# Optimization experiments

Measured on AMD Instinct MI355X. Metric: run time of the kernel, lower is better.

## Reference

```python
import jax, jax.numpy as jnp
import numpy as np

N_NODES = 50000
N_EDGES = 600000
EMB_DIM = 128
NUM_LAYERS = 5
NUM_ELEM = 118
NUM_CHIR = 4
NUM_BOND_TYPE = 4
NUM_BOND_DIR = 3
BN_EPS = 1e-5


def _xavier(key, shape):
    fan_in, fan_out = shape[0], shape[1]
    limit = np.sqrt(6.0 / (fan_in + fan_out))
    return jax.random.uniform(key, shape, jnp.float32, -limit, limit)


def setup_inputs() -> dict:
    key = jax.random.key(0)
    ks = jax.random.split(key, 12)
    x = jax.random.randint(ks[0], (N_NODES, 2), 0, 4, dtype=jnp.int64)
    edge_index = jax.random.randint(ks[1], (2, N_EDGES), 0, N_NODES, dtype=jnp.int64)
    edge_attr = jax.random.randint(ks[2], (N_EDGES, 2), 0, 3, dtype=jnp.int64)
    elem_emb = _xavier(ks[3], (NUM_ELEM, EMB_DIM))
    chir_emb = _xavier(ks[4], (NUM_CHIR, EMB_DIM))
    bond_type_emb = _xavier(ks[5], (NUM_BOND_TYPE, EMB_DIM))
    bond_dir_emb = _xavier(ks[6], (NUM_BOND_DIR, EMB_DIM))
    # shared GINEConv MLP: Linear(D, 2D) -> ReLU -> Linear(2D, D)
    W1 = _xavier(ks[7], (EMB_DIM, 2 * EMB_DIM))
    b1 = jnp.zeros((2 * EMB_DIM,), jnp.float32)
    W2 = _xavier(ks[8], (2 * EMB_DIM, EMB_DIM))
    b2 = jnp.zeros((EMB_DIM,), jnp.float32)
    # per-layer BatchNorm affine params
    bn_gamma = jnp.ones((NUM_LAYERS, EMB_DIM), jnp.float32)
    bn_beta = jnp.zeros((NUM_LAYERS, EMB_DIM), jnp.float32)
    return {
        "x": x, "edge_index": edge_index, "edge_attr": edge_attr,
        "elem_emb": elem_emb, "chir_emb": chir_emb,
        "bond_type_emb": bond_type_emb, "bond_dir_emb": bond_dir_emb,
        "W1": W1, "b1": b1, "W2": W2, "b2": b2,
        "bn_gamma": bn_gamma, "bn_beta": bn_beta,
    }


def reference(x, edge_index, edge_attr, elem_emb, chir_emb,
              bond_type_emb, bond_dir_emb, W1, b1, W2, b2,
              bn_gamma, bn_beta):
    # input embeddings
    h = elem_emb[x[:, 0]] + chir_emb[x[:, 1]]                    # [N, D]
    e = bond_type_emb[edge_attr[:, 0]] + bond_dir_emb[edge_attr[:, 1]]  # [E, D]
    src, dst = edge_index[0], edge_index[1]
    n = h.shape[0]
    num_layers = bn_gamma.shape[0]
    for layer in range(num_layers):  # conv weights shared across layers
        # GINEConv: msg = relu(x_j + edge_attr), scatter-add, eps=0
        msg = jax.nn.relu(h[src] + e)                            # [E, D]
        agg = jax.ops.segment_sum(msg, dst, num_segments=n)      # [N, D]
        z = h + agg
        out = jax.nn.relu(z @ W1 + b1) @ W2 + b2                 # [N, D]
        # BatchNorm1d (training mode: batch stats, biased variance)
        mean = out.mean(axis=0)
        var = out.var(axis=0)
        out = (out - mean) * jax.lax.rsqrt(var + BN_EPS) * bn_gamma[layer] + bn_beta[layer]
        h = out if layer == num_layers - 1 else jax.nn.relu(out)
    return h
```

## Files before the change

### kernel.cpp

```cpp
#include <hip/hip_runtime.h>

typedef _Float16 f16;
typedef _Float16 f16x8 __attribute__((ext_vector_type(8)));
typedef _Float16 h2 __attribute__((ext_vector_type(2)));
typedef float f32x4 __attribute__((ext_vector_type(4)));
typedef unsigned short u16;
typedef unsigned int u32;

__device__ __forceinline__ float bf2f(u16 b) {
  union { u32 u; float f; } t; t.u = ((u32)b) << 16; return t.f;
}
__device__ __forceinline__ u16 f2bf(float f) {
  union { float f; u32 u; } t; t.f = f;
  u32 u = t.u;
  return (u16)((u + 0x7FFFu + ((u >> 16) & 1u)) >> 16);
}
__device__ __forceinline__ u16 f2h_bits(float f) {
  f16 h = (f16)f;
  union { f16 h; u16 u; } t; t.h = h; return t.u;
}
__device__ __forceinline__ float2 up2(u32 p) {
  union { u32 u; f16 h[2]; } t; t.u = p;
  float2 r; r.x = (float)t.h[0]; r.y = (float)t.h[1]; return r;
}
__device__ __forceinline__ u32 pk2(float x, float y) {
  return (u32)f2h_bits(x) | ((u32)f2h_bits(y) << 16);
}
__device__ __forceinline__ h2 asH2(u32 u) {
  union { u32 u; h2 h; } t; t.u = u; return t.h;
}
__device__ __forceinline__ h2 relu2(h2 a) {
#if __has_builtin(__builtin_elementwise_max)
  h2 z = {(_Float16)0, (_Float16)0};
  return __builtin_elementwise_max(a, z);
#else
  h2 r;
  r.x = a.x > (_Float16)0 ? a.x : (_Float16)0;
  r.y = a.y > (_Float16)0 ? a.y : (_Float16)0;
  return r;
#endif
}

__global__ void k_detect(const u16* __restrict__ elemRaw, const int* __restrict__ eiRaw,
                         int* __restrict__ dflags) {
  __shared__ int bad, nzOdd;
  if (threadIdx.x == 0) { bad = 0; nzOdd = 0; }
  __syncthreads();
  int myBad = 0;
  for (int i = threadIdx.x; i < 4096; i += 256) {
    float v = bf2f(elemRaw[i]);
    if (!(v > -0.2f && v < 0.2f)) myBad++;
  }
  if (myBad) atomicAdd(&bad, myBad);
  int myNz = 0;
  for (int i = threadIdx.x; i < 1024; i += 256)
    if (eiRaw[2 * i + 1] != 0) myNz++;
  if (myNz) atomicAdd(&nzOdd, myNz);
  __syncthreads();
  if (threadIdx.x == 0) {
    dflags[0] = (bad == 0) ? 1 : 0;
    dflags[1] = (nzOdd > 16) ? 1 : 0;
  }
}

__global__ void k_canary(u32* __restrict__ out, const int* __restrict__ dflags,
                         int out_size, u32 pBf, u32 pF32) {
  int isbf = dflags[0];
  int words = isbf ? (out_size >> 1) : out_size;
  int i = blockIdx.x * 256 + threadIdx.x;
  if (i < words) out[i] = isbf ? pBf : pF32;
}

__global__ void k_zero(int* counts, float* stats, int NPad) {
  int i = blockIdx.x * blockDim.x + threadIdx.x;
  if (i < NPad) counts[i] = 0;
  else if (i < NPad + 1280) stats[i - NPad] = 0.f;
}

__global__ void k_cvt(const int* __restrict__ xR, const int* __restrict__ eiR,
                      const int* __restrict__ eaR,
                      const u16* e0, const u16* e1, const u16* e2, const u16* e3,
                      const u16* e4, const u16* e5, const u16* e6, const u16* e7,
                      const u16* e8, const u16* e9,
                      const int* __restrict__ dflags,
                      int* __restrict__ x32, int* __restrict__ ei32, int* __restrict__ combo,
                      int* __restrict__ counts, float* __restrict__ dst,
                      int N, int E, int intBlocks) {
  if ((int)blockIdx.x < intBlocks) {
    int pi = blockIdx.x * 256 + threadIdx.x;
    int nPairs = N + 2 * E;
    if (pi >= nPairs) return;
    int is32 = dflags[1];
    const int* src; int local; int kind;
    if (pi < N) { src = xR; local = pi; kind = 0; }
    else if (pi < N + E) { src = eiR; local = pi - N; kind = 1; }
    else { src = eaR; local = pi - N - E; kind = 2; }
    int j0 = 2 * local;
    int v0, v1;
    if (is32) { int2 v = *(const int2*)(src + j0); v0 = v.x; v1 = v.y; }
    else      { int4 v = *(const int4*)(src + 2 * j0); v0 = v.x; v1 = v.z; }
    if (kind == 0) { x32[j0] = v0; x32[j0 + 1] = v1; }
    else if (kind == 1) {
      ei32[j0] = v0; ei32[j0 + 1] = v1;
      if (j0 >= E) {
        atomicAdd(&counts[v0], 1);
        atomicAdd(&counts[v1], 1);
      }
    } else {
      combo[local] = v0 * 3 + v1;
    }
  } else {
    int i = (blockIdx.x - intBlocks) * 256 + threadIdx.x;
    if (i >= 83712) return;
    int isbf = dflags[0];
    const u16* src; int j;
    if      (i < 15104) { src = e0; j = i; }
    else if (i < 15616) { src = e1; j = i - 15104; }
    else if (i < 16128) { src = e2; j = i - 15616; }
    else if (i < 16512) { src = e3; j = i - 16128; }
    else if (i < 49280) { src = e4; j = i - 16512; }
    else if (i < 49536) { src = e5; j = i - 49280; }
    else if (i < 82304) { src = e6; j = i - 49536; }
    else if (i < 82432) { src = e7; j = i - 82304; }
    else if (i < 83072) { src = e8; j = i - 82432; }
    else                { src = e9; j = i - 83072; }
    dst[i] = isbf ? bf2f(src[j]) : ((const float*)src)[j];
  }
}

__global__ void k_chunksum(const int* __restrict__ counts, int* __restrict__ bsum) {
  int tid = threadIdx.x, lane = tid & 63, w = tid >> 6;
  const int4* c4 = (const int4*)(counts + blockIdx.x * 1024);
  int4 v = c4[tid];
  int s = v.x + v.y + v.z + v.w;
#pragma unroll
  for (int d = 1; d < 64; d <<= 1) s += __shfl_xor(s, d);
  __shared__ int ws[4];
  if (lane == 0) ws[w] = s;
  __syncthreads();
  if (tid == 0) bsum[blockIdx.x] = ws[0] + ws[1] + ws[2] + ws[3];
}

__global__ void k_chunkscan(const int* __restrict__ bsum, int* __restrict__ boff,
                            int* __restrict__ row_start, int N, int nCh) {
  int t = threadIdx.x;
  int v = (t < nCh) ? bsum[t] : 0;
  int incl = v;
#pragma unroll
  for (int d = 1; d < 64; d <<= 1) { int tmp = __shfl_up(incl, d); if (t >= d) incl += tmp; }
  boff[t] = incl - v;
  if (t == 63) row_start[N] = incl;
}

__global__ void k_scanapply(const int* __restrict__ counts, const int* __restrict__ boff,
                            int* __restrict__ row_start, int* __restrict__ cursor, int N) {
  int tid = threadIdx.x, lane = tid & 63, w = tid >> 6;
  int base = blockIdx.x * 1024 + tid * 4;
  int4 v = *(const int4*)(counts + base);
  int tsum = v.x + v.y + v.z + v.w;
  int incl = tsum;
#pragma unroll
  for (int d = 1; d < 64; d <<= 1) { int tmp = __shfl_up(incl, d); if (lane >= d) incl += tmp; }
  __shared__ int ws[4];
  if (lane == 63) ws[w] = incl;
  __syncthreads();
  int woff = 0;
  for (int j = 0; j < w; ++j) woff += ws[j];
  int excl = boff[blockIdx.x] + woff + incl - tsum;
  int e0 = excl, e1 = excl + v.x, e2 = e1 + v.y, e3 = e2 + v.z;
  if (base < N)     { row_start[base] = e0;     cursor[base] = e0; }
  if (base + 1 < N) { row_start[base + 1] = e1; cursor[base + 1] = e1; }
  if (base + 2 < N) { row_start[base + 2] = e2; cursor[base + 2] = e2; }
  if (base + 3 < N) { row_start[base + 3] = e3; cursor[base + 3] = e3; }
}

__global__ void k_scatter(const int* __restrict__ ei, const int* __restrict__ combo,
                          int* cursor, int* packed, int E) {
  int e = blockIdx.x * blockDim.x + threadIdx.x;
  if (e >= E) return;
  int s = ei[e], d = ei[E + e];
  int cb = combo[e];
  int pos = atomicAdd(&cursor[d], 1);
  packed[pos] = s | (cb << 20);
}

__global__ void k_prep(const float* __restrict__ cflt, const int* __restrict__ x,
                       u16* W1T, u16* W2T, u32* __restrict__ tblC,
                       u32* __restrict__ hb, int N, int wtBlocks) {
  if ((int)blockIdx.x < wtBlocks) {
    const float* W1 = cflt + 16512;
    const float* W2 = cflt + 49536;
    const float* bt = cflt + 15616;
    const float* bd = cflt + 16128;
    int g = blockIdx.x * 256 + threadIdx.x;
    int k1 = g >> 8, n1 = g & 255;
    W1T[n1 * 128 + k1] = f2h_bits(W1[g]);
    int k2 = g >> 7, n2 = g & 127;
    W2T[n2 * 256 + k2] = f2h_bits(W2[g]);
    if (g < 768) {
      int combo = g >> 6, l = g & 63, c0 = l * 2;
      int a0 = combo / 3, a1 = combo - a0 * 3;
      tblC[g] = pk2(bt[a0 * 128 + c0] + bd[a1 * 128 + c0],
                    bt[a0 * 128 + c0 + 1] + bd[a1 * 128 + c0 + 1]);
    }
  } else {
    const float* elem = cflt;
    const float* chir = cflt + 15104;
    int b = blockIdx.x - wtBlocks;
    int wv = (int)(threadIdx.x >> 6);
    int lane = threadIdx.x & 63;
    int node = b * 4 + wv;
    if (node >= N) return;
    int x0 = x[node * 2], x1 = x[node * 2 + 1];
    int c0 = lane * 2;
    float vx = elem[x0 * 128 + c0] + chir[x1 * 128 + c0];
    float vy = elem[x0 * 128 + c0 + 1] + chir[x1 * 128 + c0 + 1];
    hb[(size_t)node * 64 + lane] = pk2(vx, vy);
  }
}

__global__ __launch_bounds__(256) void k_agg(
    const u32* __restrict__ hb, const int* __restrict__ row_start,
    const int* __restrict__ packed, const u32* __restrict__ tblC,
    u32* __restrict__ z, int N, int Mpad) {
  __shared__ u32 tbl[12 * 64];
  for (int idx = threadIdx.x; idx < 768; idx += 256) tbl[idx] = tblC[idx];
  __syncthreads();
  int wv = __builtin_amdgcn_readfirstlane((int)(threadIdx.x >> 6));
  int lane = threadIdx.x & 63;
  int node = blockIdx.x * 4 + wv;
  if (node >= Mpad) return;
  if (node >= N) { z[(size_t)node * 64 + lane] = 0u; return; }
  float2 sv = up2(hb[(size_t)node * 64 + lane]);
  float accx = sv.x, accy = sv.y;
  int s_ = row_start[node], e_ = row_start[node + 1];
  int p = s_;
  for (; p + 4 <= e_; p += 4) {
    int k0 = packed[p], k1 = packed[p + 1], k2 = packed[p + 2], k3 = packed[p + 3];
    u32 r0 = hb[(size_t)(k0 & 0xFFFFF) * 64 + lane];
    u32 r1 = hb[(size_t)(k1 & 0xFFFFF) * 64 + lane];
    u32 r2 = hb[(size_t)(k2 & 0xFFFFF) * 64 + lane];
    u32 r3 = hb[(size_t)(k3 & 0xFFFFF) * 64 + lane];
    u32 t0 = tbl[(k0 >> 20) * 64 + lane];
    u32 t1 = tbl[(k1 >> 20) * 64 + lane];
    u32 t2 = tbl[(k2 >> 20) * 64 + lane];
    u32 t3 = tbl[(k3 >> 20) * 64 + lane];
    h2 m0 = relu2(asH2(r0) + asH2(t0));
    h2 m1 = relu2(asH2(r1) + asH2(t1));
    h2 m2 = relu2(asH2(r2) + asH2(t2));
    h2 m3 = relu2(asH2(r3) + asH2(t3));
    accx += (float)m0.x + (float)m1.x + (float)m2.x + (float)m3.x;
    accy += (float)m0.y + (float)m1.y + (float)m2.y + (float)m3.y;
  }
  for (; p < e_; ++p) {
    int k0 = packed[p];
    u32 r0 = hb[(size_t)(k0 & 0xFFFFF) * 64 + lane];
    u32 t0 = tbl[(k0 >> 20) * 64 + lane];
    h2 m0 = relu2(asH2(r0) + asH2(t0));
    accx += (float)m0.x;
    accy += (float)m0.y;
  }
  z[(size_t)node * 64 + lane] = pk2(accx, accy);
}

__global__ __launch_bounds__(256) void k_mlp(
    const u16* __restrict__ z, const u16* __restrict__ W1T, const u16* __restrict__ W2T,
    const float* __restrict__ b1, const float* __restrict__ b2,
    u16* __restrict__ act, float* __restrict__ statsL, int N) {
  __shared__ u16 sZ[64 * 128];
  __shared__ u16 sW1[64 * 128];
  __shared__ u16 sW2[128 * 64];
  __shared__ u16 sY[64 * 64];
  __shared__ float sRed[2][2][128];

  const int tid = threadIdx.x;
  const int w = tid >> 6, lane = tid & 63;
  const int lo = lane & 15, q = lane >> 4;
  const int r0 = (w & 1) * 32;
  const int c0w = (w >> 1) * 32;
  const int n20 = (w >> 1) * 64;
  const int row0 = blockIdx.x * 64;

#pragma unroll
  for (int t = 0; t < 4; ++t) {
    int L = t * 4096 + tid * 16;
    int row = L >> 8, slot = (L >> 4) & 15;
    int kb = slot ^ (row & 15);
    int4 v = *(const int4*)((const char*)z + (size_t)(row0 + row) * 256 + kb * 16);
    *(int4*)((char*)sZ + L) = v;
  }
#pragma unroll
  for (int t = 0; t < 4; ++t) {
    int L = t * 4096 + tid * 16;
    int n = L >> 8, slot = (L >> 4) & 15;
    int kb = slot ^ (n & 15);
    *(int4*)((char*)sW1 + L) =
        *(const int4*)((const char*)W1T + (size_t)n * 256 + kb * 16);
  }
#pragma unroll
  for (int t = 0; t < 4; ++t) {
    int L = t * 4096 + tid * 16;
    int n = L >> 7, slot = (L >> 4) & 7;
    int kb = slot ^ (n & 7);
    *(int4*)((char*)sW2 + L) =
        *(const int4*)((const char*)W2T + (size_t)n * 512 + kb * 16);
  }
  __syncthreads();

  f16x8 a[4][2];
#pragma unroll
  for (int ks = 0; ks < 4; ++ks) {
    int kq = ks * 4 + q;
#pragma unroll
    for (int rt = 0; rt < 2; ++rt) {
      int row = r0 + rt * 16 + lo;
      a[ks][rt] = *(const f16x8*)(sZ + row * 128 + ((kq ^ (row & 15)) << 3));
    }
  }

  f32x4 accO[2][4] = {};
  for (int c = 0; c < 4; ++c) {
    if (c) {
      __syncthreads();
#pragma unroll
      for (int t = 0; t < 4; ++t) {
        int L = t * 4096 + tid * 16;
        int n = L >> 8, slot = (L >> 4) & 15;
        int kb = slot ^ (n & 15);
        *(int4*)((char*)sW1 + L) =
            *(const int4*)((const char*)W1T + (size_t)(c * 64 + n) * 256 + kb * 16);
      }
#pragma unroll
      for (int t = 0; t < 4; ++t) {
        int L = t * 4096 + tid * 16;
        int n = L >> 7, slot = (L >> 4) & 7;
        int kb = slot ^ (n & 7);
        *(int4*)((char*)sW2 + L) =
            *(const int4*)((const char*)W2T + (size_t)n * 512 + c * 128 + kb * 16);
      }
      __syncthreads();
    }

    f32x4 acc1[2][2] = {};
#pragma unroll
    for (int ks = 0; ks < 4; ++ks) {
      int kq = ks * 4 + q;
      f16x8 b[2];
#pragma unroll
      for (int nt = 0; nt < 2; ++nt) {
        int n = c0w + nt * 16 + lo;
        b[nt] = *(const f16x8*)(sW1 + n * 128 + ((kq ^ (n & 15)) << 3));
      }
#pragma unroll
      for (int rt = 0; rt < 2; ++rt)
#pragma unroll
        for (int nt = 0; nt < 2; ++nt)
          acc1[rt][nt] = __builtin_amdgcn_mfma_f32_16x16x32_f16(a[ks][rt], b[nt], acc1[rt][nt], 0, 0, 0);
    }

#pragma unroll
    for (int nt = 0; nt < 2; ++nt) {
      int kcol = c0w + nt * 16 + lo;
      float bias = b1[c * 64 + kcol];
#pragma unroll
      for (int rt = 0; rt < 2; ++rt)
#pragma unroll
        for (int i = 0; i < 4; ++i) {
          int m = r0 + rt * 16 + q * 4 + i;
          float v = fmaxf(acc1[rt][nt][i] + bias, 0.f);
          sY[m * 64 + (((kcol >> 3) ^ (m & 7)) << 3) + (kcol & 7)] = f2h_bits(v);
        }
    }
    __syncthreads();

#pragma unroll
    for (int ks2 = 0; ks2 < 2; ++ks2) {
      int kq = ks2 * 4 + q;
      f16x8 a2[2], bb[4];
#pragma unroll
      for (int rt = 0; rt < 2; ++rt) {
        int m = r0 + rt * 16 + lo;
        a2[rt] = *(const f16x8*)(sY + m * 64 + ((kq ^ (m & 7)) << 3));
      }
#pragma unroll
      for (int nt = 0; nt < 4; ++nt) {
        int n = n20 + nt * 16 + lo;
        bb[nt] = *(const f16x8*)(sW2 + n * 64 + ((kq ^ (n & 7)) << 3));
      }
#pragma unroll
      for (int rt = 0; rt < 2; ++rt)
#pragma unroll
        for (int nt = 0; nt < 4; ++nt)
          accO[rt][nt] = __builtin_amdgcn_mfma_f32_16x16x32_f16(a2[rt], bb[nt], accO[rt][nt], 0, 0, 0);
    }
  }

#pragma unroll
  for (int nt = 0; nt < 4; ++nt) {
    int n2 = n20 + nt * 16 + lo;
    float bias = b2[n2];
    float ssum = 0.f, ssq = 0.f;
#pragma unroll
    for (int rt = 0; rt < 2; ++rt)
#pragma unroll
      for (int i = 0; i < 4; ++i) {
        int row = row0 + r0 + rt * 16 + q * 4 + i;
        float v = accO[rt][nt][i] + bias;
        act[(size_t)row * 128 + n2] = f2h_bits(v);
        if (row < N) { ssum += v; ssq += v * v; }
      }
    ssum += __shfl_xor(ssum, 16); ssum += __shfl_xor(ssum, 32);
    ssq  += __shfl_xor(ssq, 16);  ssq  += __shfl_xor(ssq, 32);
    if (q == 0) { sRed[w & 1][0][n2] = ssum; sRed[w & 1][1][n2] = ssq; }
  }
  __syncthreads();
  {
    int col = tid & 127, which = (tid >> 7) & 1;
    atomicAdd(&statsL[which * 128 + col], sRed[0][which][col] + sRed[1][which][col]);
  }
}

__global__ __launch_bounds__(256) void k_bnapply(
    const u32* __restrict__ act, const float* __restrict__ statsL,
    const float* __restrict__ gamma, const float* __restrict__ beta,
    float invN, u32* __restrict__ hb, int N) {
  __shared__ float ssc[128], ssh[128];
  int tid = threadIdx.x;
  if (tid < 128) {
    float mean = statsL[tid] * invN;
    float var = statsL[128 + tid] * invN - mean * mean;
    float inv = rsqrtf(var + 1e-5f);
    float scv = gamma[tid] * inv;
    ssc[tid] = scv;
    ssh[tid] = beta[tid] - mean * scv;
  }
  __syncthreads();
  int total = N * 64;
  for (int i = blockIdx.x * 256 + tid; i < total; i += gridDim.x * 256) {
    int c0 = (i & 63) * 2;
    float2 v = up2(act[i]);
    float ox = fmaxf(v.x * ssc[c0] + ssh[c0], 0.f);
    float oy = fmaxf(v.y * ssc[c0 + 1] + ssh[c0 + 1], 0.f);
    hb[i] = pk2(ox, oy);
  }
}

__global__ __launch_bounds__(256) void k_final(
    const u32* __restrict__ act, const float* __restrict__ statsL,
    const float* __restrict__ gamma, const float* __restrict__ beta,
    float invN, const int* __restrict__ dflags, void* __restrict__ outv, int N) {
  __shared__ float ssc[128], ssh[128];
  int tid = threadIdx.x;
  if (tid < 128) {
    float mean = statsL[tid] * invN;
    float var = statsL[128 + tid] * invN - mean * mean;
    float inv = rsqrtf(var + 1e-5f);
    float scv = gamma[tid] * inv;
    ssc[tid] = scv;
    ssh[tid] = beta[tid] - mean * scv;
  }
  __syncthreads();
  int isbf = dflags[0];
  int total = N * 64;
  for (int i = blockIdx.x * 256 + tid; i < total; i += gridDim.x * 256) {
    int c0 = (i & 63) * 2;
    float2 v = up2(act[i]);
    float ox = v.x * ssc[c0] + ssh[c0];
    float oy = v.y * ssc[c0 + 1] + ssh[c0 + 1];
    if (isbf) ((u32*)outv)[i] = (u32)f2bf(ox) | ((u32)f2bf(oy) << 16);
    else { float2 o; o.x = ox; o.y = oy; ((float2*)outv)[i] = o; }
  }
}

extern "C" void kernel_launch(void* const* d_in, const int* in_sizes, int n_in,
                              void* d_out, int out_size, void* d_ws, size_t ws_size,
                              hipStream_t stream) {
  const int* xR  = (const int*)d_in[0];
  const int* eiR = (const int*)d_in[1];
  const int* eaR = (const int*)d_in[2];
  const u16* emR = (const u16*)d_in[3];
  const u16* chR = (const u16*)d_in[4];
  const u16* btR = (const u16*)d_in[5];
  const u16* bdR = (const u16*)d_in[6];
  const u16* W1R = (const u16*)d_in[7];
  const u16* b1R = (const u16*)d_in[8];
  const u16* W2R = (const u16*)d_in[9];
  const u16* b2R = (const u16*)d_in[10];
  const u16* gR  = (const u16*)d_in[11];
  const u16* beR = (const u16*)d_in[12];

  const int N = in_sizes[0] / 2;
  const int E = in_sizes[1] / 2;
  const int L = in_sizes[11] / 128;
  const int Mpad = ((N + 63) / 64) * 64;
  const int nCh = (N + 1023) / 1024;
  const int NPad = nCh * 1024;

  char* base = (char*)d_ws;
  size_t off = 0;
  auto take = [&](size_t bytes) -> void* {
    void* p = base + off;
    off += (bytes + 255) & ~(size_t)255;
    return p;
  };
  int*   dflags    = (int*)  take(256);
  int*   x32       = (int*)  take((size_t)2 * N * 4);
  int*   ei32      = (int*)  take((size_t)2 * E * 4);
  int*   combo     = (int*)  take((size_t)E * 4);
  float* cflt      = (float*)take(83712 * 4);
  u32*   act       = (u32*)  take((size_t)Mpad * 64 * 4);
  u32*   hb        = (u32*)  take((size_t)Mpad * 64 * 4);
  u16*   zb        = (u16*)  take((size_t)Mpad * 128 * 2);
  int*   packed    = (int*)  take((size_t)E * 4);
  int*   row_start = (int*)  take((size_t)(N + 1) * 4);
  int*   cursor    = (int*)  take((size_t)N * 4);
  int*   counts    = (int*)  take((size_t)NPad * 4);
  int*   bsum      = (int*)  take(64 * 4);
  int*   boff      = (int*)  take(64 * 4);
  float* stats     = (float*)take((size_t)L * 256 * 4);
  u16*   W1T       = (u16*)  take(32768 * 2);
  u16*   W2T       = (u16*)  take(32768 * 2);
  u32*   tblC      = (u32*)  take(768 * 4);
  const size_t need = off;
  (void)n_in;

  float* cB1 = cflt + 49280;
  float* cB2 = cflt + 82304;
  float* cGamma = cflt + 82432;
  float* cBeta = cflt + 83072;

  k_detect<<<dim3(1), dim3(256), 0, stream>>>(emR, eiR, dflags);

  if (need > ws_size) {
    k_canary<<<dim3((out_size + 255) / 256), dim3(256), 0, stream>>>(
        (u32*)d_out, dflags, out_size, 0x40004000u, 0x40000000u);
    return;
  }

  k_zero<<<dim3((NPad + 1280 + 255) / 256), dim3(256), 0, stream>>>(counts, stats, NPad);

  const int nPairs = N + 2 * E;
  const int intBlocks = (nPairs + 255) / 256;
  const int fltBlocks = (83712 + 255) / 256;
  k_cvt<<<dim3(intBlocks + fltBlocks), dim3(256), 0, stream>>>(
      xR, eiR, eaR, emR, chR, btR, bdR, W1R, b1R, W2R, b2R, gR, beR,
      dflags, x32, ei32, combo, counts, cflt, N, E, intBlocks);

  k_chunksum<<<dim3(nCh), dim3(256), 0, stream>>>(counts, bsum);
  k_chunkscan<<<dim3(1), dim3(64), 0, stream>>>(bsum, boff, row_start, N, nCh);
  k_scanapply<<<dim3(nCh), dim3(256), 0, stream>>>(counts, boff, row_start, cursor, N);
  k_scatter<<<dim3((E + 255) / 256), dim3(256), 0, stream>>>(ei32, combo, cursor, packed, E);

  const int wtBlocks = 128;
  k_prep<<<dim3(wtBlocks + (N + 3) / 4), dim3(256), 0, stream>>>(
      cflt, x32, W1T, W2T, tblC, hb, N, wtBlocks);

  const float invN = 1.0f / (float)N;
  for (int l = 0; l < L; ++l) {
    k_agg<<<dim3(Mpad / 4), dim3(256), 0, stream>>>(
        hb, row_start, packed, tblC, (u32*)zb, N, Mpad);
    k_mlp<<<dim3(Mpad / 64), dim3(256), 0, stream>>>(
        zb, W1T, W2T, cB1, cB2, (u16*)act, stats + (size_t)l * 256, N);
    if (l < L - 1) {
      k_bnapply<<<dim3(1024), dim3(256), 0, stream>>>(
          act, stats + (size_t)l * 256, cGamma + (size_t)l * 128, cBeta + (size_t)l * 128,
          invN, hb, N);
    }
  }
  k_final<<<dim3(1024), dim3(256), 0, stream>>>(
      act, stats + (size_t)(L - 1) * 256, cGamma + (size_t)(L - 1) * 128,
      cBeta + (size_t)(L - 1) * 128, invN, dflags, d_out, N);
}
```

Measured before the change: 521.5 us.

## Fuse BatchNorm apply into aggregation gather and prefetch MLP weights into registers

Removes the separate BN-apply kernel. The aggregation kernel now computes the previous layer's scale and shift and applies normalize+ReLU in fp16 to each gathered neighbour row and to the self row, with a -inf clamp on layer 0 to act as identity. This drops one full read/write pass over node features per layer and one launch, but repeats the normalization on every edge (about 12x more FMAs) and does it in half precision. Separately, the MLP kernel preloads the next weight chunk into registers while the current chunk computes, which overlaps global loads with MFMA work at the cost of extra registers.

```diff
diff --git a/kernel.cpp b/kernel.cpp
--- a/kernel.cpp
+++ b/kernel.cpp
@@ -29,14 +29,13 @@
 __device__ __forceinline__ h2 asH2(u32 u) {
   union { u32 u; h2 h; } t; t.u = u; return t.h;
 }
-__device__ __forceinline__ h2 relu2(h2 a) {
+__device__ __forceinline__ h2 maxh2(h2 a, h2 b) {
 #if __has_builtin(__builtin_elementwise_max)
-  h2 z = {(_Float16)0, (_Float16)0};
-  return __builtin_elementwise_max(a, z);
+  return __builtin_elementwise_max(a, b);
 #else
   h2 r;
-  r.x = a.x > (_Float16)0 ? a.x : (_Float16)0;
-  r.y = a.y > (_Float16)0 ? a.y : (_Float16)0;
+  r.x = a.x > b.x ? a.x : b.x;
+  r.y = a.y > b.y ? a.y : b.y;
   return r;
 #endif
 }
@@ -186,7 +185,7 @@
 
 __global__ void k_prep(const float* __restrict__ cflt, const int* __restrict__ x,
                        u16* W1T, u16* W2T, u32* __restrict__ tblC,
-                       u32* __restrict__ hb, int N, int wtBlocks) {
+                       u32* __restrict__ act, int N, int wtBlocks) {
   if ((int)blockIdx.x < wtBlocks) {
     const float* W1 = cflt + 16512;
     const float* W2 = cflt + 49536;
@@ -215,48 +214,70 @@
     int c0 = lane * 2;
     float vx = elem[x0 * 128 + c0] + chir[x1 * 128 + c0];
     float vy = elem[x0 * 128 + c0 + 1] + chir[x1 * 128 + c0 + 1];
-    hb[(size_t)node * 64 + lane] = pk2(vx, vy);
+    act[(size_t)node * 64 + lane] = pk2(vx, vy);
   }
 }
 
 __global__ __launch_bounds__(256) void k_agg(
-    const u32* __restrict__ hb, const int* __restrict__ row_start,
+    const u32* __restrict__ act, const int* __restrict__ row_start,
     const int* __restrict__ packed, const u32* __restrict__ tblC,
+    const float* __restrict__ statsPrev, const float* __restrict__ gammaPrev,
+    const float* __restrict__ betaPrev, float invN, int l0,
     u32* __restrict__ z, int N, int Mpad) {
-  __shared__ u32 tbl[12 * 64];
-  for (int idx = threadIdx.x; idx < 768; idx += 256) tbl[idx] = tblC[idx];
+  __shared__ u32 tbl[768];
+  __shared__ u32 sscp[64], sshp[64];
+  int tid = threadIdx.x;
+  for (int idx = tid; idx < 768; idx += 256) tbl[idx] = tblC[idx];
+  if (tid < 64) {
+    float sc0 = 1.f, sc1 = 1.f, sh0 = 0.f, sh1 = 0.f;
+    if (!l0) {
+      int c0 = tid * 2;
+      float m0 = statsPrev[c0] * invN, m1 = statsPrev[c0 + 1] * invN;
+      float v0 = statsPrev[128 + c0] * invN - m0 * m0;
+      float v1 = statsPrev[128 + c0 + 1] * invN - m1 * m1;
+      float i0 = rsqrtf(v0 + 1e-5f), i1 = rsqrtf(v1 + 1e-5f);
+      sc0 = gammaPrev[c0] * i0; sc1 = gammaPrev[c0 + 1] * i1;
+      sh0 = betaPrev[c0] - m0 * sc0; sh1 = betaPrev[c0 + 1] - m1 * sc1;
+    }
+    sscp[tid] = pk2(sc0, sc1);
+    sshp[tid] = pk2(sh0, sh1);
+  }
   __syncthreads();
   int wv = __builtin_amdgcn_readfirstlane((int)(threadIdx.x >> 6));
   int lane = threadIdx.x & 63;
   int node = blockIdx.x * 4 + wv;
   if (node >= Mpad) return;
   if (node >= N) { z[(size_t)node * 64 + lane] = 0u; return; }
-  float2 sv = up2(hb[(size_t)node * 64 + lane]);
-  float accx = sv.x, accy = sv.y;
+  u32 limu = l0 ? 0xFC00FC00u : 0u;
+  h2 sc2 = asH2(sscp[lane]), sh2 = asH2(sshp[lane]);
+  h2 lim = asH2(limu), zero2 = asH2(0u);
+  h2 aa = asH2(act[(size_t)node * 64 + lane]);
+  h2 tt = maxh2(aa * sc2 + sh2, lim);
+  float accx = (float)tt.x, accy = (float)tt.y;
   int s_ = row_start[node], e_ = row_start[node + 1];
   int p = s_;
   for (; p + 4 <= e_; p += 4) {
     int k0 = packed[p], k1 = packed[p + 1], k2 = packed[p + 2], k3 = packed[p + 3];
-    u32 r0 = hb[(size_t)(k0 & 0xFFFFF) * 64 + lane];
-    u32 r1 = hb[(size_t)(k1 & 0xFFFFF) * 64 + lane];
-    u32 r2 = hb[(size_t)(k2 & 0xFFFFF) * 64 + lane];
-    u32 r3 = hb[(size_t)(k3 & 0xFFFFF) * 64 + lane];
+    u32 r0 = act[(size_t)(k0 & 0xFFFFF) * 64 + lane];
+    u32 r1 = act[(size_t)(k1 & 0xFFFFF) * 64 + lane];
+    u32 r2 = act[(size_t)(k2 & 0xFFFFF) * 64 + lane];
+    u32 r3 = act[(size_t)(k3 & 0xFFFFF) * 64 + lane];
     u32 t0 = tbl[(k0 >> 20) * 64 + lane];
     u32 t1 = tbl[(k1 >> 20) * 64 + lane];
     u32 t2 = tbl[(k2 >> 20) * 64 + lane];
     u32 t3 = tbl[(k3 >> 20) * 64 + lane];
-    h2 m0 = relu2(asH2(r0) + asH2(t0));
-    h2 m1 = relu2(asH2(r1) + asH2(t1));
-    h2 m2 = relu2(asH2(r2) + asH2(t2));
-    h2 m3 = relu2(asH2(r3) + asH2(t3));
+    h2 m0 = maxh2(maxh2(asH2(r0) * sc2 + sh2, lim) + asH2(t0), zero2);
+    h2 m1 = maxh2(maxh2(asH2(r1) * sc2 + sh2, lim) + asH2(t1), zero2);
+    h2 m2 = maxh2(maxh2(asH2(r2) * sc2 + sh2, lim) + asH2(t2), zero2);
+    h2 m3 = maxh2(maxh2(asH2(r3) * sc2 + sh2, lim) + asH2(t3), zero2);
     accx += (float)m0.x + (float)m1.x + (float)m2.x + (float)m3.x;
     accy += (float)m0.y + (float)m1.y + (float)m2.y + (float)m3.y;
   }
   for (; p < e_; ++p) {
     int k0 = packed[p];
-    u32 r0 = hb[(size_t)(k0 & 0xFFFFF) * 64 + lane];
+    u32 r0 = act[(size_t)(k0 & 0xFFFFF) * 64 + lane];
     u32 t0 = tbl[(k0 >> 20) * 64 + lane];
-    h2 m0 = relu2(asH2(r0) + asH2(t0));
+    h2 m0 = maxh2(maxh2(asH2(r0) * sc2 + sh2, lim) + asH2(t0), zero2);
     accx += (float)m0.x;
     accy += (float)m0.y;
   }
@@ -281,64 +302,61 @@
   const int n20 = (w >> 1) * 64;
   const int row0 = blockIdx.x * 64;
 
+  const char* W1b = (const char*)W1T;
+  const char* W2b = (const char*)W2T;
+  int L_[4], b1o[4], b2o[4];
 #pragma unroll
   for (int t = 0; t < 4; ++t) {
     int L = t * 4096 + tid * 16;
+    L_[t] = L;
+    int n1 = L >> 8, s1 = (L >> 4) & 15;
+    b1o[t] = n1 * 256 + (s1 ^ (n1 & 15)) * 16;
+    int n2 = L >> 7, s2 = (L >> 4) & 7;
+    b2o[t] = n2 * 512 + (s2 ^ (n2 & 7)) * 16;
+  }
+  int4 rW1[4], rW2[4];
+#pragma unroll
+  for (int t = 0; t < 4; ++t) {
+    rW1[t] = *(const int4*)(W1b + b1o[t]);
+    rW2[t] = *(const int4*)(W2b + b2o[t]);
+  }
+#pragma unroll
+  for (int t = 0; t < 4; ++t) {
+    int L = L_[t];
     int row = L >> 8, slot = (L >> 4) & 15;
     int kb = slot ^ (row & 15);
     int4 v = *(const int4*)((const char*)z + (size_t)(row0 + row) * 256 + kb * 16);
     *(int4*)((char*)sZ + L) = v;
   }
-#pragma unroll
-  for (int t = 0; t < 4; ++t) {
-    int L = t * 4096 + tid * 16;
-    int n = L >> 8, slot = (L >> 4) & 15;
-    int kb = slot ^ (n & 15);
-    *(int4*)((char*)sW1 + L) =
-        *(const int4*)((const char*)W1T + (size_t)n * 256 + kb * 16);
-  }
-#pragma unroll
-  for (int t = 0; t < 4; ++t) {
-    int L = t * 4096 + tid * 16;
-    int n = L >> 7, slot = (L >> 4) & 7;
-    int kb = slot ^ (n & 7);
-    *(int4*)((char*)sW2 + L) =
-        *(const int4*)((const char*)W2T + (size_t)n * 512 + kb * 16);
-  }
-  __syncthreads();
 
   f16x8 a[4][2];
-#pragma unroll
-  for (int ks = 0; ks < 4; ++ks) {
-    int kq = ks * 4 + q;
-#pragma unroll
-    for (int rt = 0; rt < 2; ++rt) {
-      int row = r0 + rt * 16 + lo;
-      a[ks][rt] = *(const f16x8*)(sZ + row * 128 + ((kq ^ (row & 15)) << 3));
-    }
-  }
-
   f32x4 accO[2][4] = {};
+#pragma unroll
   for (int c = 0; c < 4; ++c) {
-    if (c) {
-      __syncthreads();
+    if (c) __syncthreads();
+#pragma unroll
+    for (int t = 0; t < 4; ++t) {
+      *(int4*)((char*)sW1 + L_[t]) = rW1[t];
+      *(int4*)((char*)sW2 + L_[t]) = rW2[t];
+    }
+    __syncthreads();
+    if (c < 3) {
 #pragma unroll
       for (int t = 0; t < 4; ++t) {
-        int L = t * 4096 + tid * 16;
-        int n = L >> 8, slot = (L >> 4) & 15;
-        int kb = slot ^ (n & 15);
-        *(int4*)((char*)sW1 + L) =
-            *(const int4*)((const char*)W1T + (size_t)(c * 64 + n) * 256 + kb * 16);
-      }
-#pragma unroll
-      for (int t = 0; t < 4; ++t) {
-        int L = t * 4096 + tid * 16;
-        int n = L >> 7, slot = (L >> 4) & 7;
-        int kb = slot ^ (n & 7);
-        *(int4*)((char*)sW2 + L) =
-            *(const int4*)((const char*)W2T + (size_t)n * 512 + c * 128 + kb * 16);
-      }
-      __syncthreads();
+        rW1[t] = *(const int4*)(W1b + (c + 1) * 16384 + b1o[t]);
+        rW2[t] = *(const int4*)(W2b + (c + 1) * 128 + b2o[t]);
+      }
+    }
+    if (c == 0) {
+#pragma unroll
+      for (int ks = 0; ks < 4; ++ks) {
+        int kq = ks * 4 + q;
+#pragma unroll
+        for (int rt = 0; rt < 2; ++rt) {
+          int row = r0 + rt * 16 + lo;
+          a[ks][rt] = *(const f16x8*)(sZ + row * 128 + ((kq ^ (row & 15)) << 3));
+        }
+      }
     }
 
     f32x4 acc1[2][2] = {};
@@ -417,31 +435,6 @@
   {
     int col = tid & 127, which = (tid >> 7) & 1;
     atomicAdd(&statsL[which * 128 + col], sRed[0][which][col] + sRed[1][which][col]);
-  }
-}
-
-__global__ __launch_bounds__(256) void k_bnapply(
-    const u32* __restrict__ act, const float* __restrict__ statsL,
-    const float* __restrict__ gamma, const float* __restrict__ beta,
-    float invN, u32* __restrict__ hb, int N) {
-  __shared__ float ssc[128], ssh[128];
-  int tid = threadIdx.x;
-  if (tid < 128) {
-    float mean = statsL[tid] * invN;
-    float var = statsL[128 + tid] * invN - mean * mean;
-    float inv = rsqrtf(var + 1e-5f);
-    float scv = gamma[tid] * inv;
-    ssc[tid] = scv;
-    ssh[tid] = beta[tid] - mean * scv;
-  }
-  __syncthreads();
-  int total = N * 64;
-  for (int i = blockIdx.x * 256 + tid; i < total; i += gridDim.x * 256) {
-    int c0 = (i & 63) * 2;
-    float2 v = up2(act[i]);
-    float ox = fmaxf(v.x * ssc[c0] + ssh[c0], 0.f);
-    float oy = fmaxf(v.y * ssc[c0 + 1] + ssh[c0 + 1], 0.f);
-    hb[i] = pk2(ox, oy);
   }
 }
 
@@ -509,7 +502,6 @@
   int*   combo     = (int*)  take((size_t)E * 4);
   float* cflt      = (float*)take(83712 * 4);
   u32*   act       = (u32*)  take((size_t)Mpad * 64 * 4);
-  u32*   hb        = (u32*)  take((size_t)Mpad * 64 * 4);
   u16*   zb        = (u16*)  take((size_t)Mpad * 128 * 2);
   int*   packed    = (int*)  take((size_t)E * 4);
   int*   row_start = (int*)  take((size_t)(N + 1) * 4);
@@ -553,19 +545,17 @@
 
   const int wtBlocks = 128;
   k_prep<<<dim3(wtBlocks + (N + 3) / 4), dim3(256), 0, stream>>>(
-      cflt, x32, W1T, W2T, tblC, hb, N, wtBlocks);
+      cflt, x32, W1T, W2T, tblC, act, N, wtBlocks);
 
   const float invN = 1.0f / (float)N;
   for (int l = 0; l < L; ++l) {
+    int lp = (l > 0) ? (l - 1) : 0;
     k_agg<<<dim3(Mpad / 4), dim3(256), 0, stream>>>(
-        hb, row_start, packed, tblC, (u32*)zb, N, Mpad);
+        act, row_start, packed, tblC,
+        stats + (size_t)lp * 256, cGamma + (size_t)lp * 128, cBeta + (size_t)lp * 128,
+        invN, (l == 0) ? 1 : 0, (u32*)zb, N, Mpad);
     k_mlp<<<dim3(Mpad / 64), dim3(256), 0, stream>>>(
         zb, W1T, W2T, cB1, cB2, (u16*)act, stats + (size_t)l * 256, N);
-    if (l < L - 1) {
-      k_bnapply<<<dim3(1024), dim3(256), 0, stream>>>(
-          act, stats + (size_t)l * 256, cGamma + (size_t)l * 128, cBeta + (size_t)l * 128,
-          invN, hb, N);
-    }
   }
   k_final<<<dim3(1024), dim3(256), 0, stream>>>(
       act, stats + (size_t)(L - 1) * 256, cGamma + (size_t)(L - 1) * 128,
```

Measured after the change: 603.3 us. 1.16x slower.

## Restructure MLP kernel: per-wave 16-row tiles, weights read directly from global

Applied to the files above, without the earlier changes.

The fused MLP kernel now gives each wave 16 whole rows and has it compute all output columns, keeping the hidden activation in a per-wave shared-memory slice. W1 and W2 fragments are loaded straight from global memory (relying on L1/L2 caching) instead of being staged through shared memory. This removes the block-wide barriers and shared-memory staging inside the chunk loop and cuts LDS usage, which may raise occupancy. In exchange each wave issues many more uncoalesced-per-row global weight loads, so the kernel leans on cache bandwidth and latency.

```diff
diff --git a/kernel.cpp b/kernel.cpp
--- a/kernel.cpp
+++ b/kernel.cpp
@@ -223,7 +223,7 @@
     const u32* __restrict__ hb, const int* __restrict__ row_start,
     const int* __restrict__ packed, const u32* __restrict__ tblC,
     u32* __restrict__ z, int N, int Mpad) {
-  __shared__ u32 tbl[12 * 64];
+  __shared__ u32 tbl[768];
   for (int idx = threadIdx.x; idx < 768; idx += 256) tbl[idx] = tblC[idx];
   __syncthreads();
   int wv = __builtin_amdgcn_readfirstlane((int)(threadIdx.x >> 6));
@@ -268,17 +268,12 @@
     const float* __restrict__ b1, const float* __restrict__ b2,
     u16* __restrict__ act, float* __restrict__ statsL, int N) {
   __shared__ u16 sZ[64 * 128];
-  __shared__ u16 sW1[64 * 128];
-  __shared__ u16 sW2[128 * 64];
-  __shared__ u16 sY[64 * 64];
-  __shared__ float sRed[2][2][128];
+  __shared__ u16 sYp[4][16 * 64];
+  __shared__ float sRed[4][2][128];
 
   const int tid = threadIdx.x;
   const int w = tid >> 6, lane = tid & 63;
   const int lo = lane & 15, q = lane >> 4;
-  const int r0 = (w & 1) * 32;
-  const int c0w = (w >> 1) * 32;
-  const int n20 = (w >> 1) * 64;
   const int row0 = blockIdx.x * 64;
 
 #pragma unroll
@@ -286,137 +281,86 @@
     int L = t * 4096 + tid * 16;
     int row = L >> 8, slot = (L >> 4) & 15;
     int kb = slot ^ (row & 15);
-    int4 v = *(const int4*)((const char*)z + (size_t)(row0 + row) * 256 + kb * 16);
-    *(int4*)((char*)sZ + L) = v;
-  }
-#pragma unroll
-  for (int t = 0; t < 4; ++t) {
-    int L = t * 4096 + tid * 16;
-    int n = L >> 8, slot = (L >> 4) & 15;
-    int kb = slot ^ (n & 15);
-    *(int4*)((char*)sW1 + L) =
-        *(const int4*)((const char*)W1T + (size_t)n * 256 + kb * 16);
-  }
-#pragma unroll
-  for (int t = 0; t < 4; ++t) {
-    int L = t * 4096 + tid * 16;
-    int n = L >> 7, slot = (L >> 4) & 7;
-    int kb = slot ^ (n & 7);
-    *(int4*)((char*)sW2 + L) =
-        *(const int4*)((const char*)W2T + (size_t)n * 512 + kb * 16);
-  }
-  __syncthreads();
-
-  f16x8 a[4][2];
+    *(int4*)((char*)sZ + L) =
+        *(const int4*)((const char*)z + (size_t)(row0 + row) * 256 + kb * 16);
+  }
+  __syncthreads();
+
+  const int rw = w * 16 + lo;
+  f16x8 a1[4];
 #pragma unroll
   for (int ks = 0; ks < 4; ++ks) {
     int kq = ks * 4 + q;
-#pragma unroll
-    for (int rt = 0; rt < 2; ++rt) {
-      int row = r0 + rt * 16 + lo;
-      a[ks][rt] = *(const f16x8*)(sZ + row * 128 + ((kq ^ (row & 15)) << 3));
-    }
-  }
-
-  f32x4 accO[2][4] = {};
+    a1[ks] = *(const f16x8*)(sZ + rw * 128 + ((kq ^ lo) << 3));
+  }
+
+  u16* myY = sYp[w];
+  f32x4 accO[8] = {};
+#pragma unroll
   for (int c = 0; c < 4; ++c) {
-    if (c) {
-      __syncthreads();
-#pragma unroll
-      for (int t = 0; t < 4; ++t) {
-        int L = t * 4096 + tid * 16;
-        int n = L >> 8, slot = (L >> 4) & 15;
-        int kb = slot ^ (n & 15);
-        *(int4*)((char*)sW1 + L) =
-            *(const int4*)((const char*)W1T + (size_t)(c * 64 + n) * 256 + kb * 16);
-      }
-#pragma unroll
-      for (int t = 0; t < 4; ++t) {
-        int L = t * 4096 + tid * 16;
-        int n = L >> 7, slot = (L >> 4) & 7;
-        int kb = slot ^ (n & 7);
-        *(int4*)((char*)sW2 + L) =
-            *(const int4*)((const char*)W2T + (size_t)n * 512 + c * 128 + kb * 16);
-      }
-      __syncthreads();
-    }
-
-    f32x4 acc1[2][2] = {};
+    f32x4 acc1[4] = {};
 #pragma unroll
     for (int ks = 0; ks < 4; ++ks) {
       int kq = ks * 4 + q;
-      f16x8 b[2];
-#pragma unroll
-      for (int nt = 0; nt < 2; ++nt) {
-        int n = c0w + nt * 16 + lo;
-        b[nt] = *(const f16x8*)(sW1 + n * 128 + ((kq ^ (n & 15)) << 3));
+      f16x8 b[4];
+#pragma unroll
+      for (int nt = 0; nt < 4; ++nt) {
+        int n = c * 64 + nt * 16 + lo;
+        b[nt] = *(const f16x8*)((const char*)W1T + (size_t)n * 256 + kq * 16);
       }
 #pragma unroll
-      for (int rt = 0; rt < 2; ++rt)
-#pragma unroll
-        for (int nt = 0; nt < 2; ++nt)
-          acc1[rt][nt] = __builtin_amdgcn_mfma_f32_16x16x32_f16(a[ks][rt], b[nt], acc1[rt][nt], 0, 0, 0);
-    }
-
-#pragma unroll
-    for (int nt = 0; nt < 2; ++nt) {
-      int kcol = c0w + nt * 16 + lo;
-      float bias = b1[c * 64 + kcol];
-#pragma unroll
-      for (int rt = 0; rt < 2; ++rt)
-#pragma unroll
-        for (int i = 0; i < 4; ++i) {
-          int m = r0 + rt * 16 + q * 4 + i;
-          float v = fmaxf(acc1[rt][nt][i] + bias, 0.f);
-          sY[m * 64 + (((kcol >> 3) ^ (m & 7)) << 3) + (kcol & 7)] = f2h_bits(v);
-        }
-    }
-    __syncthreads();
-
+      for (int nt = 0; nt < 4; ++nt)
+        acc1[nt] = __builtin_amdgcn_mfma_f32_16x16x32_f16(a1[ks], b[nt], acc1[nt], 0, 0, 0);
+    }
+#pragma unroll
+    for (int nt = 0; nt < 4; ++nt) {
+      int ycol = nt * 16 + lo;
+      float bias = b1[c * 64 + ycol];
+#pragma unroll
+      for (int i = 0; i < 4; ++i) {
+        int m = q * 4 + i;
+        float v = fmaxf(acc1[nt][i] + bias, 0.f);
+        myY[m * 64 + (((ycol >> 3) ^ (m & 7)) << 3) + (ycol & 7)] = f2h_bits(v);
+      }
+    }
 #pragma unroll
     for (int ks2 = 0; ks2 < 2; ++ks2) {
-      int kq = ks2 * 4 + q;
-      f16x8 a2[2], bb[4];
-#pragma unroll
-      for (int rt = 0; rt < 2; ++rt) {
-        int m = r0 + rt * 16 + lo;
-        a2[rt] = *(const f16x8*)(sY + m * 64 + ((kq ^ (m & 7)) << 3));
+      int kq2 = ks2 * 4 + q;
+      f16x8 a2 = *(const f16x8*)(myY + lo * 64 + ((kq2 ^ (lo & 7)) << 3));
+      f16x8 bb[8];
+#pragma unroll
+      for (int nt = 0; nt < 8; ++nt) {
+        int n2 = nt * 16 + lo;
+        bb[nt] = *(const f16x8*)((const char*)W2T + (size_t)n2 * 512 + c * 128 + kq2 * 16);
       }
 #pragma unroll
-      for (int nt = 0; nt < 4; ++nt) {
-        int n = n20 + nt * 16 + lo;
-        bb[nt] = *(const f16x8*)(sW2 + n * 64 + ((kq ^ (n & 7)) << 3));
-      }
-#pragma unroll
-      for (int rt = 0; rt < 2; ++rt)
-#pragma unroll
-        for (int nt = 0; nt < 4; ++nt)
-          accO[rt][nt] = __builtin_amdgcn_mfma_f32_16x16x32_f16(a2[rt], bb[nt], accO[rt][nt], 0, 0, 0);
-    }
-  }
-
-#pragma unroll
-  for (int nt = 0; nt < 4; ++nt) {
-    int n2 = n20 + nt * 16 + lo;
+      for (int nt = 0; nt < 8; ++nt)
+        accO[nt] = __builtin_amdgcn_mfma_f32_16x16x32_f16(a2, bb[nt], accO[nt], 0, 0, 0);
+    }
+  }
+
+#pragma unroll
+  for (int nt = 0; nt < 8; ++nt) {
+    int n2 = nt * 16 + lo;
     float bias = b2[n2];
     float ssum = 0.f, ssq = 0.f;
 #pragma unroll
-    for (int rt = 0; rt < 2; ++rt)
-#pragma unroll
-      for (int i = 0; i < 4; ++i) {
-        int row = row0 + r0 + rt * 16 + q * 4 + i;
-        float v = accO[rt][nt][i] + bias;
-        act[(size_t)row * 128 + n2] = f2h_bits(v);
-        if (row < N) { ssum += v; ssq += v * v; }
-      }
+    for (int i = 0; i < 4; ++i) {
+      int row = row0 + w * 16 + q * 4 + i;
+      float v = accO[nt][i] + bias;
+      act[(size_t)row * 128 + n2] = f2h_bits(v);
+      if (row < N) { ssum += v; ssq += v * v; }
+    }
     ssum += __shfl_xor(ssum, 16); ssum += __shfl_xor(ssum, 32);
     ssq  += __shfl_xor(ssq, 16);  ssq  += __shfl_xor(ssq, 32);
-    if (q == 0) { sRed[w & 1][0][n2] = ssum; sRed[w & 1][1][n2] = ssq; }
+    if (q == 0) { sRed[w][0][n2] = ssum; sRed[w][1][n2] = ssq; }
   }
   __syncthreads();
   {
     int col = tid & 127, which = (tid >> 7) & 1;
-    atomicAdd(&statsL[which * 128 + col], sRed[0][which][col] + sRed[1][which][col]);
+    float s = sRed[0][which][col] + sRed[1][which][col] +
+              sRed[2][which][col] + sRed[3][which][col];
+    atomicAdd(&statsL[which * 128 + col], s);
   }
 }
 
```

Result: slower. 747.5 us (+43.3%).
